# Kernel tuning notes

Measured on AMD Instinct MI355X. Metric: run time of the kernel, lower is better.

## Reference

```python
import jax, jax.numpy as jnp
import numpy as np

N_NODES = 100000
N_EDGES = 1600000
D = 32
K = 3  # Chebyshev kernels
NEG_SLOPE = 0.2


def setup_inputs() -> dict:
    key = jax.random.key(0)
    ks = jax.random.split(key, 10)
    s = 1.0 / np.sqrt(D)
    return {
        "u": jax.random.normal(ks[0], (N_NODES, D), jnp.float32),
        "lambda_max": jnp.full((1,), 2.0, jnp.float32),
        "edge_src": jax.random.randint(ks[1], (N_EDGES,), 0, N_NODES, jnp.int32),
        "edge_dst": jax.random.randint(ks[2], (N_EDGES,), 0, N_NODES, jnp.int32),
        "cheb_W": jax.random.normal(ks[3], (K * D, D), jnp.float32) * s,
        "cheb_b": jnp.zeros((D,), jnp.float32),
        "src_W": jax.random.normal(ks[4], (D, D), jnp.float32) * s,
        "src_b": jnp.zeros((D,), jnp.float32),
        "dst_W": jax.random.normal(ks[5], (D, D), jnp.float32) * s,
        "dst_b": jnp.zeros((D,), jnp.float32),
        "attn": jax.random.normal(ks[6], (1, D), jnp.float32) * s,  # (heads=1, D)
    }


def reference(u, lambda_max, edge_src, edge_dst, cheb_W, cheb_b,
              src_W, src_b, dst_W, dst_b, attn):
    N = u.shape[0]
    # in-degrees (DGL: clamp(min=1) ** -0.5)
    deg = jnp.zeros((N,), u.dtype).at[edge_dst].add(1.0)
    Dinv = jnp.clip(deg, 1.0, None) ** -0.5  # (N,)

    def unnL(x):  # D^{-1/2} A D^{-1/2} x  via copy_u->sum message passing
        m = (x * Dinv[:, None])[edge_src]                       # (E, D)
        agg = jax.ops.segment_sum(m, edge_dst, num_segments=N)  # (N, D)
        return agg * Dinv[:, None]

    # --- ChebConv ---
    re_norm = 2.0 / lambda_max  # (1,) broadcast over all nodes
    X0 = u
    Xt = [X0]
    X1 = X0
    if K > 1:
        h = unnL(X0)
        X1 = -re_norm * h + X0 * (re_norm - 1.0)
        Xt.append(X1)
    for _ in range(2, K):
        h = unnL(X1)
        Xi = -2.0 * re_norm * h + X1 * (2.0 * (re_norm - 1.0)) - X0
        Xt.append(Xi)
        X0, X1 = X1, Xi
    Xcat = jnp.concatenate(Xt, axis=1)                 # (N, K*D)
    hc = jax.nn.relu(Xcat @ cheb_W + cheb_b)           # (N, D), DGL default activation=relu

    # --- GATv2Conv (heads=1) ---
    H = attn.shape[0]
    fsrc = (hc @ src_W + src_b).reshape(N, H, -1)      # (N, H, D)
    fdst = (hc @ dst_W + dst_b).reshape(N, H, -1)
    e = jax.nn.leaky_relu(fsrc[edge_src] + fdst[edge_dst], NEG_SLOPE)  # (E, H, D)
    logits = jnp.einsum('ehd,hd->eh', e, attn)         # (E, H)
    mx = jax.ops.segment_max(logits, edge_dst, num_segments=N)
    mx = jnp.where(jnp.isfinite(mx), mx, 0.0)
    ex = jnp.exp(logits - mx[edge_dst])
    den = jax.ops.segment_sum(ex, edge_dst, num_segments=N)
    a = ex / jnp.where(den > 0, den, 1.0)[edge_dst]    # edge softmax over dst groups
    msg = fsrc[edge_src] * a[:, :, None]               # (E, H, D)
    out = jax.ops.segment_sum(msg, edge_dst, num_segments=N)  # (N, H, D)
    return out.squeeze(1)
```

## Files before the change

### kernel.cpp

```cpp
#include <hip/hip_runtime.h>
#include <hip/hip_bf16.h>


typedef unsigned short u16;

#define DD 32
#define NEG_SLOPE 0.2f
#define BLK 256
#define TILE 4096
#define CB_SHIFT 8
#define CB_NODES 256
#define SRC_BITS 17

#define OFF_CHEBW 0
#define OFF_CHEBB 3072
#define OFF_SRCW  3104
#define OFF_SRCB  4128
#define OFF_DSTW  4160
#define OFF_DSTB  5184
#define OFF_ATTN  5216
#define OFF_LMAX  5248
#define W_TOTAL   5249

#define F_U     0
#define F_CHEBW 1
#define F_CHEBB 2
#define F_SRCW  3
#define F_SRCB  4
#define F_DSTW  5
#define F_DSTB  6
#define F_ATTN  7
#define F_LMAX  8
#define N_FLAGS 9

__device__ __forceinline__ float bh2f(u16 h) {
    return __uint_as_float(((unsigned)h) << 16);
}
__device__ __forceinline__ float rdin(const void* p, long long i, int f32f) {
    return f32f ? ((const float*)p)[i] : bh2f(((const u16*)p)[i]);
}
__device__ __forceinline__ float4 rd4(const void* p, long long row, int q, int f32f) {
    if (f32f) return ((const float4*)p)[row * 8 + q];
    ushort4 h = ((const ushort4*)p)[row * 8 + q];
    return make_float4(bh2f(h.x), bh2f(h.y), bh2f(h.z), bh2f(h.w));
}
__device__ __forceinline__ float lrelu(float x) { return fmaxf(x, NEG_SLOPE * x); }

__device__ __forceinline__ int plaus(u16 h) {
    if ((h & 0x7FFFu) == 0) return 1;
    unsigned e = (h >> 7) & 0xFF;
    return (e >= 0x60 && e <= 0x8F) ? 1 : 0;
}

__global__ __launch_bounds__(BLK) void k_prep(
        const void* u, const void* chebW, const void* chebB, const void* srcW,
        const void* srcB, const void* dstW, const void* dstB, const void* attn,
        const void* lmax, int n0, int n7, int* __restrict__ flags,
        float* __restrict__ wsW, unsigned* __restrict__ Mabs,
        unsigned* __restrict__ gcnt) {
    __shared__ int cEven, cEvenZ, cOddNZ, fl;
    const void* ptrs[N_FLAGS] = {u, chebW, chebB, srcW, srcB, dstW, dstB, attn, lmax};
    const int   ns[N_FLAGS]   = {n0, 3072, 32, 1024, 32, 1024, 32, n7, 1};
    const int   offs[N_FLAGS] = {0, OFF_CHEBW, OFF_CHEBB, OFF_SRCW, OFF_SRCB,
                                 OFF_DSTW, OFF_DSTB, OFF_ATTN, OFF_LMAX};
    int a = blockIdx.x;
    if (a >= N_FLAGS) return;
    int t = threadIdx.x;
    const u16* h = (const u16*)ptrs[a];
    int n = ns[a];
    if (t == 0) { cEven = 0; cEvenZ = 0; cOddNZ = 0; }
    if (a == 0) {
        if (t < 32) Mabs[t] = 0u;
        if (t == 32) *gcnt = 0u;
    }
    __syncthreads();
    if (n == 1) {
        if (t == 0) {
            u16 v = h[0];
            fl = ((v & 0x7FFFu) == 0 || !plaus(v)) ? 1 : 0;
            flags[a] = fl;
        }
    } else {
        int nprobe = n >> 1;
        if (nprobe > 64) nprobe = 64;
        if (t < nprobe) {
            u16 ev = h[2 * t];
            u16 od = h[2 * t + 1];
            if (plaus(ev)) atomicAdd(&cEven, 1);
            if ((ev & 0x7FFFu) == 0) atomicAdd(&cEvenZ, 1);
            if (plaus(od) && (od & 0x7FFFu) != 0) atomicAdd(&cOddNZ, 1);
        }
        __syncthreads();
        if (t == 0) {
            int bf = (cEven * 4 >= nprobe * 3);
            if (cEvenZ == nprobe && cOddNZ * 2 >= nprobe) bf = 0;
            fl = bf ? 0 : 1;
            flags[a] = fl;
        }
    }
    __syncthreads();
    if (a == 0) return;
    int f = fl;
    int cnt = ns[a];
    int doff = offs[a];
    for (int i = t; i < cnt; i += BLK)
        wsW[doff + i] = rdin(ptrs[a], i, f);
}


__global__ __launch_bounds__(BLK) void k_h1(
        const int* __restrict__ dst, unsigned* __restrict__ hist1,
        int E, int T, int NB1) {
    __shared__ unsigned lh[512];
    int tile = blockIdx.x, t = threadIdx.x;
    for (int b = t; b < 512; b += BLK) lh[b] = 0;
    __syncthreads();
    int base = tile * TILE;
    for (int i = 0; i < TILE / BLK; i++) {
        int e = base + i * BLK + t;
        if (e < E) atomicAdd(&lh[dst[e] >> CB_SHIFT], 1u);
    }
    __syncthreads();
    for (int b = t; b < NB1; b += BLK) hist1[(size_t)b * T + tile] = lh[b];
}

__global__ __launch_bounds__(BLK) void k_scA(
        unsigned* __restrict__ h, unsigned* __restrict__ bsum, int T,
        unsigned* __restrict__ row_ptr, int N, int E,
        unsigned* __restrict__ gcnt) {
    __shared__ unsigned s[BLK];
    __shared__ int lastdone;
    int b = blockIdx.x, t = threadIdx.x;
    int NB = gridDim.x;
    unsigned carry = 0;
    for (int base = 0; base < T; base += BLK) {
        int i = base + t;
        unsigned v = (i < T) ? h[(size_t)b * T + i] : 0u;
        s[t] = v;
        __syncthreads();
        for (int off = 1; off < BLK; off <<= 1) {
            unsigned a = (t >= off) ? s[t - off] : 0u;
            __syncthreads();
            s[t] += a;
            __syncthreads();
        }
        if (i < T) h[(size_t)b * T + i] = carry + s[t] - v;
        carry += s[BLK - 1];
        __syncthreads();
    }
    if (t == 0) {
        bsum[b] = carry;
        __threadfence();
        unsigned old = atomicAdd(gcnt, 1u);
        lastdone = (old == (unsigned)(NB - 1)) ? 1 : 0;
    }
    __syncthreads();
    if (!lastdone) return;
    __threadfence();
    unsigned c2 = 0;
    for (int base = 0; base < NB; base += BLK) {
        int i = base + t;
        unsigned v = (i < NB) ? bsum[i] : 0u;
        s[t] = v;
        __syncthreads();
        for (int off = 1; off < BLK; off <<= 1) {
            unsigned a = (t >= off) ? s[t - off] : 0u;
            __syncthreads();
            s[t] += a;
            __syncthreads();
        }
        if (i < NB) bsum[i] = c2 + s[t] - v;
        c2 += s[BLK - 1];
        __syncthreads();
    }
    if (t == 0) row_ptr[N] = (unsigned)E;
}

__global__ __launch_bounds__(BLK) void k_s1(
        const int* __restrict__ src, const int* __restrict__ dst,
        const unsigned* __restrict__ off1, const unsigned* __restrict__ bsum,
        unsigned* __restrict__ tmp, int E, int T, int NB1) {
    __shared__ unsigned cur[512];
    int tile = blockIdx.x, t = threadIdx.x;
    for (int b = t; b < NB1; b += BLK)
        cur[b] = off1[(size_t)b * T + tile] + bsum[b];
    __syncthreads();
    int base = tile * TILE;
    for (int i = 0; i < TILE / BLK; i++) {
        int e = base + i * BLK + t;
        if (e < E) {
            int d = dst[e];
            unsigned pos = atomicAdd(&cur[d >> CB_SHIFT], 1u);
            tmp[pos] = ((unsigned)(d & (CB_NODES - 1)) << SRC_BITS) | (unsigned)src[e];
        }
    }
}

__global__ __launch_bounds__(BLK) void k_p2(
        const unsigned* __restrict__ tmp, const unsigned* __restrict__ bsum,
        unsigned* __restrict__ row_ptr, float* __restrict__ dinv,
        int* __restrict__ srcs, int N, int E, int T, int NB1) {
    __shared__ unsigned hist[CB_NODES], cur[CB_NODES], ssc[BLK];
    int b = blockIdx.x, t = threadIdx.x;
    int nodeBase = b << CB_SHIFT;
    unsigned lo = bsum[b];
    unsigned hi = (b + 1 < NB1) ? bsum[b + 1] : (unsigned)E;
    hist[t] = 0;
    __syncthreads();
    for (unsigned e = lo + t; e < hi; e += BLK)
        atomicAdd(&hist[tmp[e] >> SRC_BITS], 1u);
    __syncthreads();
    unsigned v = hist[t];
    ssc[t] = v;
    __syncthreads();
    for (int off = 1; off < BLK; off <<= 1) {
        unsigned a = (t >= off) ? ssc[t - off] : 0u;
        __syncthreads();
        ssc[t] += a;
        __syncthreads();
    }
    unsigned ex = ssc[t] - v;
    cur[t] = ex;
    int node = nodeBase + t;
    if (node < N) {
        row_ptr[node] = lo + ex;
        unsigned c = v;
        if (c < 1u) c = 1u;
        dinv[node] = rsqrtf((float)c);
    }
    __syncthreads();
    for (unsigned e = lo + t; e < hi; e += BLK) {
        unsigned p = tmp[e];
        unsigned pos = lo + atomicAdd(&cur[p >> SRC_BITS], 1u);
        srcs[pos] = (int)(p & ((1u << SRC_BITS) - 1u));
    }
}


__global__ __launch_bounds__(BLK) void k_unnl1(
        const void* __restrict__ u, const int* __restrict__ flags,
        const float* __restrict__ dinv, const unsigned* __restrict__ row_ptr,
        const int* __restrict__ srcs, const float* __restrict__ wsW,
        float* __restrict__ X1, int N) {
    int node = (blockIdx.x * BLK + threadIdx.x) >> 3;
    if (node >= N) return;
    int q = threadIdx.x & 7;
    int f = flags[F_U];
    int base = (int)row_ptr[node], end = (int)row_ptr[node + 1];
    float4 acc = make_float4(0.f, 0.f, 0.f, 0.f);
    for (int i = base; i < end; i += 4) {
        int e1 = i + 1, e2 = i + 2, e3 = i + 3;
        int s0 = srcs[i];
        int s1 = srcs[min(e1, end - 1)];
        int s2 = srcs[min(e2, end - 1)];
        int s3 = srcs[min(e3, end - 1)];
        float dv0 = dinv[s0], dv1 = dinv[s1], dv2 = dinv[s2], dv3 = dinv[s3];
        if (e1 >= end) dv1 = 0.f;
        if (e2 >= end) dv2 = 0.f;
        if (e3 >= end) dv3 = 0.f;
        float4 x0 = rd4(u, s0, q, f);
        float4 x1 = rd4(u, s1, q, f);
        float4 x2 = rd4(u, s2, q, f);
        float4 x3 = rd4(u, s3, q, f);
        acc.x += x0.x * dv0 + x1.x * dv1 + x2.x * dv2 + x3.x * dv3;
        acc.y += x0.y * dv0 + x1.y * dv1 + x2.y * dv2 + x3.y * dv3;
        acc.z += x0.z * dv0 + x1.z * dv1 + x2.z * dv2 + x3.z * dv3;
        acc.w += x0.w * dv0 + x1.w * dv1 + x2.w * dv2 + x3.w * dv3;
    }
    float rn = 2.0f / wsW[OFF_LMAX];
    float dn = dinv[node];
    float4 x0 = rd4(u, node, q, f);
    float4 r;
    r.x = -rn * (acc.x * dn) + x0.x * (rn - 1.f);
    r.y = -rn * (acc.y * dn) + x0.y * (rn - 1.f);
    r.z = -rn * (acc.z * dn) + x0.z * (rn - 1.f);
    r.w = -rn * (acc.w * dn) + x0.w * (rn - 1.f);
    ((float4*)X1)[(size_t)node * 8 + q] = r;
}

__global__ __launch_bounds__(BLK) void k_unnl2(
        const void* __restrict__ u, const int* __restrict__ flags,
        const float* __restrict__ X1, const float* __restrict__ dinv,
        const unsigned* __restrict__ row_ptr, const int* __restrict__ srcs,
        const float* __restrict__ wsW, float* __restrict__ X2, int N) {
    int node = (blockIdx.x * BLK + threadIdx.x) >> 3;
    if (node >= N) return;
    int q = threadIdx.x & 7;
    int base = (int)row_ptr[node], end = (int)row_ptr[node + 1];
    float4 acc = make_float4(0.f, 0.f, 0.f, 0.f);
    for (int i = base; i < end; i += 4) {
        int e1 = i + 1, e2 = i + 2, e3 = i + 3;
        int s0 = srcs[i];
        int s1 = srcs[min(e1, end - 1)];
        int s2 = srcs[min(e2, end - 1)];
        int s3 = srcs[min(e3, end - 1)];
        float dv0 = dinv[s0], dv1 = dinv[s1], dv2 = dinv[s2], dv3 = dinv[s3];
        if (e1 >= end) dv1 = 0.f;
        if (e2 >= end) dv2 = 0.f;
        if (e3 >= end) dv3 = 0.f;
        float4 x0 = ((const float4*)X1)[(size_t)s0 * 8 + q];
        float4 x1 = ((const float4*)X1)[(size_t)s1 * 8 + q];
        float4 x2 = ((const float4*)X1)[(size_t)s2 * 8 + q];
        float4 x3 = ((const float4*)X1)[(size_t)s3 * 8 + q];
        acc.x += x0.x * dv0 + x1.x * dv1 + x2.x * dv2 + x3.x * dv3;
        acc.y += x0.y * dv0 + x1.y * dv1 + x2.y * dv2 + x3.y * dv3;
        acc.z += x0.z * dv0 + x1.z * dv1 + x2.z * dv2 + x3.z * dv3;
        acc.w += x0.w * dv0 + x1.w * dv1 + x2.w * dv2 + x3.w * dv3;
    }
    float rn = 2.0f / wsW[OFF_LMAX];
    float dn = dinv[node];
    float4 x0 = rd4(u, node, q, flags[F_U]);
    float4 x1 = ((const float4*)X1)[(size_t)node * 8 + q];
    float4 r;
    r.x = -2.f * rn * (acc.x * dn) + x1.x * (2.f * (rn - 1.f)) - x0.x;
    r.y = -2.f * rn * (acc.y * dn) + x1.y * (2.f * (rn - 1.f)) - x0.y;
    r.z = -2.f * rn * (acc.z * dn) + x1.z * (2.f * (rn - 1.f)) - x0.z;
    r.w = -2.f * rn * (acc.w * dn) + x1.w * (2.f * (rn - 1.f)) - x0.w;
    ((float4*)X2)[(size_t)node * 8 + q] = r;
}

__global__ __launch_bounds__(BLK) void k_cfsd(
        const void* __restrict__ u, const int* __restrict__ flags,
        const float* __restrict__ X1, const float* __restrict__ X2,
        const float* __restrict__ wsW, float* __restrict__ fsrc,
        float* __restrict__ fdst, unsigned* __restrict__ Mabs, int N) {
    __shared__ float sW[3072], sWs[1024], sWd[1024];
    __shared__ float sb[32], sbs[32], sbd[32];
    __shared__ unsigned mloc[32];
    int t = threadIdx.x;
    for (int i = t; i < 3072; i += BLK) sW[i] = wsW[OFF_CHEBW + i];
    for (int i = t; i < 1024; i += BLK) {
        sWs[i] = wsW[OFF_SRCW + i];
        sWd[i] = wsW[OFF_DSTW + i];
    }
    if (t < 32) {
        sb[t]  = wsW[OFF_CHEBB + t];
        sbs[t] = wsW[OFF_SRCB + t];
        sbd[t] = wsW[OFF_DSTB + t];
        mloc[t] = 0u;
    }
    __syncthreads();
    int f = flags[F_U];
    float mabs = 0.f;
    int n = blockIdx.x * BLK + t;
    if (n < N) {
        long long row = (long long)n;
        float acc[32];
#pragma unroll
        for (int j = 0; j < 32; j++) acc[j] = sb[j];
        for (int i4 = 0; i4 < 8; i4++) {
            float4 x = rd4(u, row, i4, f);
            const float* w = &sW[i4 * 128];
#pragma unroll
            for (int j = 0; j < 32; j++) acc[j] = fmaf(x.x, w[j], acc[j]);
#pragma unroll
            for (int j = 0; j < 32; j++) acc[j] = fmaf(x.y, w[32 + j], acc[j]);
#pragma unroll
            for (int j = 0; j < 32; j++) acc[j] = fmaf(x.z, w[64 + j], acc[j]);
#pragma unroll
            for (int j = 0; j < 32; j++) acc[j] = fmaf(x.w, w[96 + j], acc[j]);
        }
        for (int i4 = 0; i4 < 8; i4++) {
            float4 x = ((const float4*)X1)[row * 8 + i4];
            const float* w = &sW[1024 + i4 * 128];
#pragma unroll
            for (int j = 0; j < 32; j++) acc[j] = fmaf(x.x, w[j], acc[j]);
#pragma unroll
            for (int j = 0; j < 32; j++) acc[j] = fmaf(x.y, w[32 + j], acc[j]);
#pragma unroll
            for (int j = 0; j < 32; j++) acc[j] = fmaf(x.z, w[64 + j], acc[j]);
#pragma unroll
            for (int j = 0; j < 32; j++) acc[j] = fmaf(x.w, w[96 + j], acc[j]);
        }
        for (int i4 = 0; i4 < 8; i4++) {
            float4 x = ((const float4*)X2)[row * 8 + i4];
            const float* w = &sW[2048 + i4 * 128];
#pragma unroll
            for (int j = 0; j < 32; j++) acc[j] = fmaf(x.x, w[j], acc[j]);
#pragma unroll
            for (int j = 0; j < 32; j++) acc[j] = fmaf(x.y, w[32 + j], acc[j]);
#pragma unroll
            for (int j = 0; j < 32; j++) acc[j] = fmaf(x.z, w[64 + j], acc[j]);
#pragma unroll
            for (int j = 0; j < 32; j++) acc[j] = fmaf(x.w, w[96 + j], acc[j]);
        }
#pragma unroll
        for (int j = 0; j < 32; j++) acc[j] = fmaxf(acc[j], 0.f);
        float as[32], ad[32];
#pragma unroll
        for (int j = 0; j < 32; j++) { as[j] = sbs[j]; ad[j] = sbd[j]; }
#pragma unroll
        for (int i = 0; i < 32; i++) {
            float hv = acc[i];
            const float* ws = &sWs[i * 32];
            const float* wd = &sWd[i * 32];
#pragma unroll
            for (int j = 0; j < 32; j++) {
                as[j] = fmaf(hv, ws[j], as[j]);
                ad[j] = fmaf(hv, wd[j], ad[j]);
            }
        }
        float4* fs4 = (float4*)(fsrc + row * 32);
        float4* fd4 = (float4*)(fdst + row * 32);
#pragma unroll
        for (int i4 = 0; i4 < 8; i4++) {
            fs4[i4] = make_float4(as[4 * i4], as[4 * i4 + 1], as[4 * i4 + 2], as[4 * i4 + 3]);
            fd4[i4] = make_float4(ad[4 * i4], ad[4 * i4 + 1], ad[4 * i4 + 2], ad[4 * i4 + 3]);
        }
#pragma unroll
        for (int j = 0; j < 32; j++) mabs = fmaxf(mabs, fabsf(as[j]));
    }
    atomicMax(&mloc[t & 31], __float_as_uint(mabs));
    __syncthreads();
    if (t < 32) atomicMax(&Mabs[t], mloc[t]);
}

__global__ __launch_bounds__(BLK) void k_gat(
        const float* __restrict__ fsrc, const float* __restrict__ fdst,
        const unsigned* __restrict__ row_ptr, const int* __restrict__ srcs,
        const float* __restrict__ wsW, const unsigned* __restrict__ Mabs,
        float* __restrict__ out, int N) {
    int node = (blockIdx.x * BLK + threadIdx.x) >> 3;
    if (node >= N) return;
    int q = threadIdx.x & 7;
    int base = (int)row_ptr[node], end = (int)row_ptr[node + 1];
    if (base == end) {
        ((float4*)out)[(size_t)node * 8 + q] = make_float4(0.f, 0.f, 0.f, 0.f);
        return;
    }
    float4 fd = ((const float4*)fdst)[(size_t)node * 8 + q];
    float4 at = ((const float4*)(wsW + OFF_ATTN))[q];
    float4 mb = ((const float4*)Mabs)[q];
    float kp = (mb.x + fabsf(fd.x)) * fabsf(at.x) +
               (mb.y + fabsf(fd.y)) * fabsf(at.y) +
               (mb.z + fabsf(fd.z)) * fabsf(at.z) +
               (mb.w + fabsf(fd.w)) * fabsf(at.w);
    kp += __shfl_xor(kp, 1);
    kp += __shfl_xor(kp, 2);
    kp += __shfl_xor(kp, 4);
    float K = kp;
    float4 acc = make_float4(0.f, 0.f, 0.f, 0.f);
    float den = 0.f;
    for (int i = base; i < end; i += 2) {
        int e1 = i + 1;
        int s0 = srcs[i];
        int s1 = srcs[min(e1, end - 1)];
        float4 fs0 = ((const float4*)fsrc)[(size_t)s0 * 8 + q];
        float4 fs1 = ((const float4*)fsrc)[(size_t)s1 * 8 + q];
        float v0 = lrelu(fs0.x + fd.x) * at.x + lrelu(fs0.y + fd.y) * at.y +
                   lrelu(fs0.z + fd.z) * at.z + lrelu(fs0.w + fd.w) * at.w;
        float v1 = lrelu(fs1.x + fd.x) * at.x + lrelu(fs1.y + fd.y) * at.y +
                   lrelu(fs1.z + fd.z) * at.z + lrelu(fs1.w + fd.w) * at.w;
        v0 += __shfl_xor(v0, 1);  v1 += __shfl_xor(v1, 1);
        v0 += __shfl_xor(v0, 2);  v1 += __shfl_xor(v1, 2);
        v0 += __shfl_xor(v0, 4);  v1 += __shfl_xor(v1, 4);
        float w0 = __expf(v0 - K);
        float w1 = (e1 < end) ? __expf(v1 - K) : 0.f;
        acc.x += fs0.x * w0 + fs1.x * w1;
        acc.y += fs0.y * w0 + fs1.y * w1;
        acc.z += fs0.z * w0 + fs1.z * w1;
        acc.w += fs0.w * w0 + fs1.w * w1;
        den += w0 + w1;
    }
    float inv = 1.f / (den > 0.f ? den : 1.f);
    ((float4*)out)[(size_t)node * 8 + q] =
        make_float4(acc.x * inv, acc.y * inv, acc.z * inv, acc.w * inv);
}

extern "C" void kernel_launch(void* const* d_in, const int* in_sizes, int n_in,
                              void* d_out, int out_size, void* d_ws, size_t ws_size,
                              hipStream_t stream) {
    const void* u     = d_in[0];
    const void* lmax  = d_in[1];
    const int*  esrc  = (const int*)d_in[2];
    const int*  edst  = (const int*)d_in[3];
    const void* chebW = d_in[4];
    const void* chebB = d_in[5];
    const void* srcW  = d_in[6];
    const void* srcB  = d_in[7];
    const void* dstW  = d_in[8];
    const void* dstB  = d_in[9];
    const void* attn  = d_in[10];

    const int ND = in_sizes[0];
    const int N  = ND / DD;
    const int E  = in_sizes[2];

    const int NB1 = (N + CB_NODES - 1) >> CB_SHIFT;
    const int T   = (E + TILE - 1) / TILE;
    const int M   = NB1 * T;

    float* ws   = (float*)d_ws;
    float* X1   = ws;
    float* X2   = ws + (size_t)ND;
    unsigned* tmp = (unsigned*)(ws + 2 * (size_t)ND);
    int*   srcs = (int*)(tmp + E);
    unsigned* hist1   = (unsigned*)(srcs + E);
    unsigned* row_ptr = hist1 + M;
    float*    dinv    = (float*)(row_ptr + (N + 1));
    unsigned* bsum    = (unsigned*)(dinv + N);
    float*    wsW     = (float*)(((uintptr_t)(bsum + NB1) + 15) & ~(uintptr_t)15);
    int*      flags   = (int*)(wsW + W_TOTAL);
    unsigned* Mabs    = (unsigned*)(((uintptr_t)(flags + N_FLAGS) + 15) & ~(uintptr_t)15);
    unsigned* gcnt    = Mabs + 32;
    float*    out     = (float*)d_out;

    auto gb = [](long long n, int b) { return (unsigned)((n + b - 1) / b); };

    k_prep<<<N_FLAGS, BLK, 0, stream>>>(u, chebW, chebB, srcW, srcB, dstW, dstB,
                                        attn, lmax, ND, DD, flags, wsW, Mabs, gcnt);

    k_h1<<<T, BLK, 0, stream>>>(edst, hist1, E, T, NB1);
    k_scA<<<NB1, BLK, 0, stream>>>(hist1, bsum, T, row_ptr, N, E, gcnt);
    k_s1<<<T, BLK, 0, stream>>>(esrc, edst, hist1, bsum, tmp, E, T, NB1);
    k_p2<<<NB1, BLK, 0, stream>>>(tmp, bsum, row_ptr, dinv, srcs, N, E, T, NB1);

    k_unnl1<<<gb((long long)N * 8, BLK), BLK, 0, stream>>>(u, flags, dinv, row_ptr,
                                                           srcs, wsW, X1, N);
    k_unnl2<<<gb((long long)N * 8, BLK), BLK, 0, stream>>>(u, flags, X1, dinv, row_ptr,
                                                           srcs, wsW, X2, N);

    k_cfsd<<<gb(N, BLK), BLK, 0, stream>>>(u, flags, X1, X2, wsW, X1, X2, Mabs, N);

    k_gat<<<gb((long long)N * 8, BLK), BLK, 0, stream>>>(X1, X2, row_ptr, srcs,
                                                         wsW, Mabs, out, N);
}
```

Measured before the change: 278.5 us.

## Remap Chebyshev/GAT projection kernel to 8 lanes per node pair

The fused Chebyshev-linear plus source/destination projection kernel previously used one thread per node, holding 32- and 64-float accumulator arrays in registers. It now assigns 8 lanes to each pair of nodes, with each lane owning 4 output columns as float4 accumulators. The hidden vector is shared across lanes with ds_swizzle broadcasts, and weights are read as float4 from shared memory. The goal is lower register pressure, higher occupancy and coalesced row loads and stores, at the cost of redundant input row reads across lanes and extra cross-lane shuffles.

```diff
diff --git a/kernel.cpp b/kernel.cpp
--- a/kernel.cpp
+++ b/kernel.cpp
@@ -51,6 +51,21 @@
     unsigned e = (h >> 7) & 0xFF;
     return (e >= 0x60 && e <= 0x8F) ? 1 : 0;
 }
+
+template<int G>
+__device__ __forceinline__ float4 bc8(float4 v) {
+    constexpr int imm = (G << 5) | 0x18;
+    float4 r;
+    r.x = __int_as_float(__builtin_amdgcn_ds_swizzle(__float_as_int(v.x), imm));
+    r.y = __int_as_float(__builtin_amdgcn_ds_swizzle(__float_as_int(v.y), imm));
+    r.z = __int_as_float(__builtin_amdgcn_ds_swizzle(__float_as_int(v.z), imm));
+    r.w = __int_as_float(__builtin_amdgcn_ds_swizzle(__float_as_int(v.w), imm));
+    return r;
+}
+
+#define FMA4(ACC, S, W) \
+    ACC.x = fmaf((S), (W).x, ACC.x); ACC.y = fmaf((S), (W).y, ACC.y); \
+    ACC.z = fmaf((S), (W).z, ACC.z); ACC.w = fmaf((S), (W).w, ACC.w)
 
 __global__ __launch_bounds__(BLK) void k_prep(
         const void* u, const void* chebW, const void* chebB, const void* srcW,
@@ -324,8 +339,8 @@
         const float* __restrict__ X1, const float* __restrict__ X2,
         const float* __restrict__ wsW, float* __restrict__ fsrc,
         float* __restrict__ fdst, unsigned* __restrict__ Mabs, int N) {
-    __shared__ float sW[3072], sWs[1024], sWd[1024];
-    __shared__ float sb[32], sbs[32], sbd[32];
+    __shared__ __align__(16) float sW[3072], sWs[1024], sWd[1024];
+    __shared__ __align__(16) float sb[32], sbs[32], sbd[32];
     __shared__ unsigned mloc[32];
     int t = threadIdx.x;
     for (int i = t; i < 3072; i += BLK) sW[i] = wsW[OFF_CHEBW + i];
@@ -341,74 +356,85 @@
     }
     __syncthreads();
     int f = flags[F_U];
+    int q = t & 7;
+    int gg = (blockIdx.x * BLK + t) >> 3;
+    long long nA = 2LL * gg, nB = nA + 1;
+    bool vA = nA < N, vB = nB < N;
+    long long rA = vA ? nA : (N - 1);
+    long long rB = vB ? nB : (N - 1);
+
+    const float4* fW = (const float4*)sW;
+    float4 accA = ((const float4*)sb)[q];
+    float4 accB = accA;
+    for (int i4 = 0; i4 < 8; i4++) {
+        float4 xa = rd4(u, rA, i4, f);
+        float4 xb = rd4(u, rB, i4, f);
+        const float4* wp = fW + i4 * 32 + q;
+        float4 w;
+        w = wp[0];  FMA4(accA, xa.x, w); FMA4(accB, xb.x, w);
+        w = wp[8];  FMA4(accA, xa.y, w); FMA4(accB, xb.y, w);
+        w = wp[16]; FMA4(accA, xa.z, w); FMA4(accB, xb.z, w);
+        w = wp[24]; FMA4(accA, xa.w, w); FMA4(accB, xb.w, w);
+    }
+    for (int i4 = 0; i4 < 8; i4++) {
+        float4 xa = ((const float4*)X1)[rA * 8 + i4];
+        float4 xb = ((const float4*)X1)[rB * 8 + i4];
+        const float4* wp = fW + 256 + i4 * 32 + q;
+        float4 w;
+        w = wp[0];  FMA4(accA, xa.x, w); FMA4(accB, xb.x, w);
+        w = wp[8];  FMA4(accA, xa.y, w); FMA4(accB, xb.y, w);
+        w = wp[16]; FMA4(accA, xa.z, w); FMA4(accB, xb.z, w);
+        w = wp[24]; FMA4(accA, xa.w, w); FMA4(accB, xb.w, w);
+    }
+    for (int i4 = 0; i4 < 8; i4++) {
+        float4 xa = ((const float4*)X2)[rA * 8 + i4];
+        float4 xb = ((const float4*)X2)[rB * 8 + i4];
+        const float4* wp = fW + 512 + i4 * 32 + q;
+        float4 w;
+        w = wp[0];  FMA4(accA, xa.x, w); FMA4(accB, xb.x, w);
+        w = wp[8];  FMA4(accA, xa.y, w); FMA4(accB, xb.y, w);
+        w = wp[16]; FMA4(accA, xa.z, w); FMA4(accB, xb.z, w);
+        w = wp[24]; FMA4(accA, xa.w, w); FMA4(accB, xb.w, w);
+    }
+    accA.x = fmaxf(accA.x, 0.f); accA.y = fmaxf(accA.y, 0.f);
+    accA.z = fmaxf(accA.z, 0.f); accA.w = fmaxf(accA.w, 0.f);
+    accB.x = fmaxf(accB.x, 0.f); accB.y = fmaxf(accB.y, 0.f);
+    accB.z = fmaxf(accB.z, 0.f); accB.w = fmaxf(accB.w, 0.f);
+
+    const float4* fWs = (const float4*)sWs;
+    const float4* fWd = (const float4*)sWd;
+    float4 asA = ((const float4*)sbs)[q];
+    float4 adA = ((const float4*)sbd)[q];
+    float4 asB = asA, adB = adA;
+#define PROJ_G(G) { \
+    float4 hA = bc8<G>(accA), hB = bc8<G>(accB); \
+    const float4* wsp = fWs + (4*(G))*8 + q; \
+    const float4* wdp = fWd + (4*(G))*8 + q; \
+    float4 w; \
+    w = wsp[0];  FMA4(asA, hA.x, w); FMA4(asB, hB.x, w); \
+    w = wsp[8];  FMA4(asA, hA.y, w); FMA4(asB, hB.y, w); \
+    w = wsp[16]; FMA4(asA, hA.z, w); FMA4(asB, hB.z, w); \
+    w = wsp[24]; FMA4(asA, hA.w, w); FMA4(asB, hB.w, w); \
+    w = wdp[0];  FMA4(adA, hA.x, w); FMA4(adB, hB.x, w); \
+    w = wdp[8];  FMA4(adA, hA.y, w); FMA4(adB, hB.y, w); \
+    w = wdp[16]; FMA4(adA, hA.z, w); FMA4(adB, hB.z, w); \
+    w = wdp[24]; FMA4(adA, hA.w, w); FMA4(adB, hB.w, w); }
+    PROJ_G(0) PROJ_G(1) PROJ_G(2) PROJ_G(3)
+    PROJ_G(4) PROJ_G(5) PROJ_G(6) PROJ_G(7)
+#undef PROJ_G
+
     float mabs = 0.f;
-    int n = blockIdx.x * BLK + t;
-    if (n < N) {
-        long long row = (long long)n;
-        float acc[32];
-#pragma unroll
-        for (int j = 0; j < 32; j++) acc[j] = sb[j];
-        for (int i4 = 0; i4 < 8; i4++) {
-            float4 x = rd4(u, row, i4, f);
-            const float* w = &sW[i4 * 128];
-#pragma unroll
-            for (int j = 0; j < 32; j++) acc[j] = fmaf(x.x, w[j], acc[j]);
-#pragma unroll
-            for (int j = 0; j < 32; j++) acc[j] = fmaf(x.y, w[32 + j], acc[j]);
-#pragma unroll
-            for (int j = 0; j < 32; j++) acc[j] = fmaf(x.z, w[64 + j], acc[j]);
-#pragma unroll
-            for (int j = 0; j < 32; j++) acc[j] = fmaf(x.w, w[96 + j], acc[j]);
-        }
-        for (int i4 = 0; i4 < 8; i4++) {
-            float4 x = ((const float4*)X1)[row * 8 + i4];
-            const float* w = &sW[1024 + i4 * 128];
-#pragma unroll
-            for (int j = 0; j < 32; j++) acc[j] = fmaf(x.x, w[j], acc[j]);
-#pragma unroll
-            for (int j = 0; j < 32; j++) acc[j] = fmaf(x.y, w[32 + j], acc[j]);
-#pragma unroll
-            for (int j = 0; j < 32; j++) acc[j] = fmaf(x.z, w[64 + j], acc[j]);
-#pragma unroll
-            for (int j = 0; j < 32; j++) acc[j] = fmaf(x.w, w[96 + j], acc[j]);
-        }
-        for (int i4 = 0; i4 < 8; i4++) {
-            float4 x = ((const float4*)X2)[row * 8 + i4];
-            const float* w = &sW[2048 + i4 * 128];
-#pragma unroll
-            for (int j = 0; j < 32; j++) acc[j] = fmaf(x.x, w[j], acc[j]);
-#pragma unroll
-            for (int j = 0; j < 32; j++) acc[j] = fmaf(x.y, w[32 + j], acc[j]);
-#pragma unroll
-            for (int j = 0; j < 32; j++) acc[j] = fmaf(x.z, w[64 + j], acc[j]);
-#pragma unroll
-            for (int j = 0; j < 32; j++) acc[j] = fmaf(x.w, w[96 + j], acc[j]);
-        }
-#pragma unroll
-        for (int j = 0; j < 32; j++) acc[j] = fmaxf(acc[j], 0.f);
-        float as[32], ad[32];
-#pragma unroll
-        for (int j = 0; j < 32; j++) { as[j] = sbs[j]; ad[j] = sbd[j]; }
-#pragma unroll
-        for (int i = 0; i < 32; i++) {
-            float hv = acc[i];
-            const float* ws = &sWs[i * 32];
-            const float* wd = &sWd[i * 32];
-#pragma unroll
-            for (int j = 0; j < 32; j++) {
-                as[j] = fmaf(hv, ws[j], as[j]);
-                ad[j] = fmaf(hv, wd[j], ad[j]);
-            }
-        }
-        float4* fs4 = (float4*)(fsrc + row * 32);
-        float4* fd4 = (float4*)(fdst + row * 32);
-#pragma unroll
-        for (int i4 = 0; i4 < 8; i4++) {
-            fs4[i4] = make_float4(as[4 * i4], as[4 * i4 + 1], as[4 * i4 + 2], as[4 * i4 + 3]);
-            fd4[i4] = make_float4(ad[4 * i4], ad[4 * i4 + 1], ad[4 * i4 + 2], ad[4 * i4 + 3]);
-        }
-#pragma unroll
-        for (int j = 0; j < 32; j++) mabs = fmaxf(mabs, fabsf(as[j]));
+    if (vA) {
+        ((float4*)fsrc)[rA * 8 + q] = asA;
+        ((float4*)fdst)[rA * 8 + q] = adA;
+        mabs = fmaxf(fmaxf(fabsf(asA.x), fabsf(asA.y)),
+                     fmaxf(fabsf(asA.z), fabsf(asA.w)));
+    }
+    if (vB) {
+        ((float4*)fsrc)[rB * 8 + q] = asB;
+        ((float4*)fdst)[rB * 8 + q] = adB;
+        mabs = fmaxf(mabs, fmaxf(fmaxf(fabsf(asB.x), fabsf(asB.y)),
+                                 fmaxf(fabsf(asB.z), fabsf(asB.w))));
     }
     atomicMax(&mloc[t & 31], __float_as_uint(mabs));
     __syncthreads();
@@ -520,7 +546,11 @@
     k_unnl2<<<gb((long long)N * 8, BLK), BLK, 0, stream>>>(u, flags, X1, dinv, row_ptr,
                                                            srcs, wsW, X2, N);
 
-    k_cfsd<<<gb(N, BLK), BLK, 0, stream>>>(u, flags, X1, X2, wsW, X1, X2, Mabs, N);
+    {
+        long long groups = (N + 1) / 2;
+        k_cfsd<<<gb(groups * 8, BLK), BLK, 0, stream>>>(u, flags, X1, X2, wsW,
+                                                        X1, X2, Mabs, N);
+    }
 
     k_gat<<<gb((long long)N * 8, BLK), BLK, 0, stream>>>(X1, X2, row_ptr, srcs,
                                                          wsW, Mabs, out, N);
```

Result: slower. 297.1 us (+6.7%).
